# Kernel tuning notes

Hardware: AMD Instinct MI355X
Metric: run time of the kernel (lower is better)

The kernel has to match this reference:

```python
import jax, jax.numpy as jnp
import numpy as np

B = 128        # graph pairs per batch
NPG = 512      # nodes per graph (equal-size graphs -> dense batch is a reshape)
D = 64         # input feature dim
DEG = 16       # avg degree
FILTERS = [64, 32, 16]
RDIM = 10      # resize_dim
CCH = 8        # conv channels per similarity image
MLP = [32, 16, 8, 4, 1]


def _make_edges(rng, n_graphs, npg, deg):
    E = n_graphs * npg * deg
    off = np.repeat(np.arange(n_graphs, dtype=np.int64) * npg, npg * deg)
    src = rng.integers(0, npg, E) + off
    dst = rng.integers(0, npg, E) + off
    return jnp.asarray(np.stack([src, dst]), dtype=jnp.int32)


def setup_inputs() -> dict:
    key = jax.random.key(0)
    ks = jax.random.split(key, 40)
    rng = np.random.default_rng(0)
    N = B * NPG
    inp = {}
    inp['x_i'] = jax.random.normal(ks[0], (N, D), jnp.float32)
    inp['x_j'] = jax.random.normal(ks[1], (N, D), jnp.float32)
    # GCN weights
    dims = [D] + FILTERS
    k = 2
    for li in range(3):
        fi, fo = dims[li], dims[li + 1]
        inp[f'gcn_w{li}'] = jax.random.normal(ks[k], (fi, fo), jnp.float32) / np.sqrt(fi); k += 1
        inp[f'gcn_b{li}'] = jnp.zeros((fo,), jnp.float32)
    # Conv filters: one Conv2d(1->CCH, 3x3, SAME) per GNN layer, OIHW kernels
    for li in range(3):
        inp[f'conv_w{li}'] = jax.random.normal(ks[k], (CCH, 1, 3, 3), jnp.float32) / 3.0; k += 1
        inp[f'conv_b{li}'] = jnp.zeros((CCH,), jnp.float32)
    # MLP (Linear-ReLU stack) + scoring layer
    mdims = [3 * CCH * RDIM * RDIM] + MLP
    for li in range(len(MLP)):
        fi, fo = mdims[li], mdims[li + 1]
        inp[f'mlp_w{li}'] = jax.random.normal(ks[k], (fi, fo), jnp.float32) / np.sqrt(fi); k += 1
        inp[f'mlp_b{li}'] = jnp.zeros((fo,), jnp.float32)
    inp['score_w'] = jax.random.normal(ks[k], (1, 1), jnp.float32); k += 1
    inp['score_b'] = jnp.zeros((1,), jnp.float32)
    # Graph structure (int constants)
    inp['edge_index_i'] = _make_edges(rng, B, NPG, DEG)
    inp['edge_index_j'] = _make_edges(rng, B, NPG, DEG)
    batch = jnp.asarray(np.repeat(np.arange(B, dtype=np.int64), NPG), dtype=jnp.int32)
    inp['batch_i'] = batch
    inp['batch_j'] = batch
    return inp


def _gcn(x, ei, w, b):
    # PyG GCNConv: A_hat = D^-1/2 (A + I) D^-1/2 ; out = A_hat (x W) + b
    src, dst = ei[0], ei[1]
    n = x.shape[0]
    xw = x @ w
    deg = jax.ops.segment_sum(jnp.ones(ei.shape[1], xw.dtype), dst, num_segments=n) + 1.0
    inv = jax.lax.rsqrt(deg)
    msg = xw[src] * (inv[src] * inv[dst])[:, None]
    agg = jax.ops.segment_sum(msg, dst, num_segments=n)
    return agg + xw * (inv * inv)[:, None] + b


def _forward(x_i, x_j, gcn_w0, gcn_b0, gcn_w1, gcn_b1, gcn_w2, gcn_b2,
             conv_w0, conv_b0, conv_w1, conv_b1, conv_w2, conv_b2,
             mlp_w0, mlp_b0, mlp_w1, mlp_b1, mlp_w2, mlp_b2, mlp_w3, mlp_b3, mlp_w4, mlp_b4,
             score_w, score_b, edge_index_i, edge_index_j):
    gws = [(gcn_w0, gcn_b0), (gcn_w1, gcn_b1), (gcn_w2, gcn_b2)]
    cvs = [(conv_w0, conv_b0), (conv_w1, conv_b1), (conv_w2, conv_b2)]
    embs = []
    for li, (w, b) in enumerate(gws):
        x_i = _gcn(x_i, edge_index_i, w, b)
        x_j = _gcn(x_j, edge_index_j, w, b)
        if li != len(gws) - 1:  # activation + dropout (eval mode -> identity)
            x_i = jax.nn.relu(x_i)
            x_j = jax.nn.relu(x_j)
        h_i = x_i.reshape(B, NPG, -1)  # to_dense_batch (equal-size graphs)
        h_j = x_j.reshape(B, NPG, -1)
        sim = jnp.einsum('bnd,bmd->bnm', h_i, h_j)  # [B, NPG, NPG]
        simr = jax.image.resize(sim, (B, RDIM, RDIM), method='bilinear', antialias=False)
        cw, cb = cvs[li]
        y = jax.lax.conv_general_dilated(simr[:, None], cw, (1, 1), 'SAME')
        y = jax.nn.relu(y + cb[None, :, None, None])  # [B, CCH, RDIM, RDIM]
        embs.append(y.reshape(B, -1))
    feat = jnp.concatenate(embs, axis=1)  # [B, 3*CCH*RDIM*RDIM]
    for w, b in [(mlp_w0, mlp_b0), (mlp_w1, mlp_b1), (mlp_w2, mlp_b2), (mlp_w3, mlp_b3), (mlp_w4, mlp_b4)]:
        feat = jax.nn.relu(feat @ w + b)
    score = jax.nn.sigmoid(feat @ score_w + score_b)
    return score.reshape(-1)


def reference(x_i, x_j, gcn_w0, gcn_b0, gcn_w1, gcn_b1, gcn_w2, gcn_b2,
              conv_w0, conv_b0, conv_w1, conv_b1, conv_w2, conv_b2,
              mlp_w0, mlp_b0, mlp_w1, mlp_b1, mlp_w2, mlp_b2, mlp_w3, mlp_b3, mlp_w4, mlp_b4,
              score_w, score_b, edge_index_i, edge_index_j, batch_i, batch_j):
    # batch_i/batch_j are implicit in the block layout (equal-size graphs)
    return _forward(x_i, x_j, gcn_w0, gcn_b0, gcn_w1, gcn_b1, gcn_w2, gcn_b2,
                    conv_w0, conv_b0, conv_w1, conv_b1, conv_w2, conv_b2,
                    mlp_w0, mlp_b0, mlp_w1, mlp_b1, mlp_w2, mlp_b2, mlp_w3, mlp_b3, mlp_w4, mlp_b4,
                    score_w, score_b, edge_index_i, edge_index_j)
```

## Files before the change

### kernel.cpp

```cpp
#include <hip/hip_runtime.h>
#include <hip/hip_fp16.h>

typedef float fvec4 __attribute__((ext_vector_type(4)));
typedef int ivec4 __attribute__((ext_vector_type(4)));

#define NN 65536
#define EE 1048576
#define BB 128
#define NPG 512
#define EPG 8192

__device__ __forceinline__ int pkrtz(float a, float b) {
  union { __half2 h; int i; } u; u.h = __floats2half2_rn(a, b); return u.i;
}
__device__ __forceinline__ float2 up2(int v) {
  union { int i; __half2 h; } u; u.i = v; return __half22float2(u.h);
}

#define ACCQ(SA, SB, w) { float2 f_; \
  f_ = up2((w)[0]); (SA)[0] += f_.x; (SA)[1] += f_.y; \
  f_ = up2((w)[1]); (SA)[2] += f_.x; (SA)[3] += f_.y; \
  f_ = up2((w)[2]); (SB)[0] += f_.x; (SB)[1] += f_.y; \
  f_ = up2((w)[3]); (SB)[2] += f_.x; (SB)[3] += f_.y; }

__device__ __forceinline__ int slot_of(int node) {
  constexpr int srows[20] = {25, 26, 76, 77, 127, 128, 178, 179, 229, 230,
                             281, 282, 332, 333, 383, 384, 434, 435, 485, 486};
  int slot = -1;
#pragma unroll
  for (int i = 0; i < 20; ++i)
    if (node == srows[i]) slot = i;
  return slot;
}
__constant__ int c_srows[20] = {25, 26, 76, 77, 127, 128, 178, 179, 229, 230,
                                281, 282, 332, 333, 383, 384, 434, 435, 485, 486};

__global__ __launch_bounds__(512)
void kA(const float* __restrict__ x_i, const float* __restrict__ x_j,
        const float* __restrict__ gw0, const float* __restrict__ gb0,
        const float* __restrict__ gw1,
        const int* __restrict__ ei, const int* __restrict__ ej,
        unsigned short* __restrict__ sidsG, unsigned int* __restrict__ packG,
        float* __restrict__ hs0, unsigned int* __restrict__ y1G) {
  __shared__ ivec4 buf[NPG * 4];
  __shared__ unsigned short sids[EPG];
  __shared__ int cnt[NPG];
  __shared__ int posb[NPG];
  __shared__ int wsum[8];
  unsigned short* const dsts = reinterpret_cast<unsigned short*>(buf);

  const int bid = blockIdx.x;
  const int half = bid & 1;
  const int sg = bid >> 1;
  const int side = sg >> 7, g = sg & 127;
  const float* __restrict__ x = side ? x_j : x_i;
  const int* __restrict__ eidx = side ? ej : ei;
  const int v = threadIdx.x;
  const int base = g * NPG, ebase = g * EPG;

  cnt[v] = 0;
  __syncthreads();
  for (int k = v; k < EPG; k += 512) {
    int d = eidx[EE + ebase + k] - base;
    dsts[k] = (unsigned short)d;
    atomicAdd(&cnt[d], 1);
  }
  __syncthreads();

  const int count = cnt[v];
  int xa = count;
  const int lane = v & 63;
#pragma unroll
  for (int d = 1; d < 64; d <<= 1) {
    int y = __shfl_up(xa, d, 64);
    if (lane >= d) xa += y;
  }
  const int wid = v >> 6;
  if (lane == 63) wsum[wid] = xa;
  __syncthreads();
  if (v == 0) {
    int a = 0;
#pragma unroll
    for (int i = 0; i < 8; ++i) { int tv = wsum[i]; wsum[i] = a; a += tv; }
  }
  __syncthreads();
  posb[v] = xa - count + wsum[wid];
  __syncthreads();

  for (int k = v; k < EPG; k += 512) {
    int lv = eidx[ebase + k] - base;
    int p = atomicAdd(&posb[dsts[k]], 1);
    sids[p] = (unsigned short)lv;
  }

  fvec4 a0[8];
#pragma unroll
  for (int q = 0; q < 8; ++q) a0[q] = fvec4{0.f, 0.f, 0.f, 0.f};
  {
    const fvec4* xv = reinterpret_cast<const fvec4*>(x + (size_t)(base + v) * 64);
    const float* w0h = gw0 + half * 32;
#pragma unroll 1
    for (int k16 = 0; k16 < 4; ++k16) {
      fvec4 xq[4];
#pragma unroll
      for (int u = 0; u < 4; ++u) xq[u] = xv[4 * k16 + u];
#pragma unroll
      for (int u = 0; u < 4; ++u) {
#pragma unroll
        for (int j = 0; j < 4; ++j) {
          const float xk = xq[u][j];
          const fvec4* wr = reinterpret_cast<const fvec4*>(w0h + (size_t)(16 * k16 + 4 * u + j) * 64);
#pragma unroll
          for (int q = 0; q < 8; ++q) a0[q] += xk * wr[q];
        }
      }
    }
  }
  __syncthreads();

  const int sgE = sg * EPG;
  if (half == 0) {
    const int* srcI = reinterpret_cast<const int*>(sids);
    int* dstI = reinterpret_cast<int*>(sidsG + sgE);
    for (int k = v; k < EPG / 2; k += 512) dstI[k] = srcI[k];
    packG[sg * NPG + v] = ((unsigned int)(posb[v] - count) << 16) | (unsigned int)count;
  }
  const float inv_v = rsqrtf((float)count + 1.0f);
  const int myKey = (v << 2) | ((v >> 1) & 3);
  fvec4 s[8];
#pragma unroll
  for (int q = 0; q < 8; ++q) s[q] = a0[q] * inv_v;
#pragma unroll
  for (int q_ = 0; q_ < 4; ++q_) {
    ivec4 w_;
    w_[0] = pkrtz(s[2 * q_][0], s[2 * q_][1]);
    w_[1] = pkrtz(s[2 * q_][2], s[2 * q_][3]);
    w_[2] = pkrtz(s[2 * q_ + 1][0], s[2 * q_ + 1][1]);
    w_[3] = pkrtz(s[2 * q_ + 1][2], s[2 * q_ + 1][3]);
    buf[myKey ^ q_] = w_;
  }
  __syncthreads();

  const int nstart = posb[v] - count;
  {
    int e = nstart;
    const int end = nstart + count;
    for (; e + 2 <= end; e += 2) {
      const int la = sids[e], lb = sids[e + 1];
      const int Ka = (la << 2) | ((la >> 1) & 3);
      const int Kb = (lb << 2) | ((lb >> 1) & 3);
      const ivec4 a0_ = buf[Ka], a1_ = buf[Ka ^ 1], a2_ = buf[Ka ^ 2], a3_ = buf[Ka ^ 3];
      const ivec4 b0_ = buf[Kb], b1_ = buf[Kb ^ 1], b2_ = buf[Kb ^ 2], b3_ = buf[Kb ^ 3];
      ACCQ(s[0], s[1], a0_) ACCQ(s[2], s[3], a1_) ACCQ(s[4], s[5], a2_) ACCQ(s[6], s[7], a3_)
      ACCQ(s[0], s[1], b0_) ACCQ(s[2], s[3], b1_) ACCQ(s[4], s[5], b2_) ACCQ(s[6], s[7], b3_)
    }
    if (e < end) {
      const int la = sids[e];
      const int Ka = (la << 2) | ((la >> 1) & 3);
      const ivec4 a0_ = buf[Ka], a1_ = buf[Ka ^ 1], a2_ = buf[Ka ^ 2], a3_ = buf[Ka ^ 3];
      ACCQ(s[0], s[1], a0_) ACCQ(s[2], s[3], a1_) ACCQ(s[4], s[5], a2_) ACCQ(s[6], s[7], a3_)
    }
  }

  const int slot = slot_of(v);
  const int hb = (side * BB + g) * 20;
  fvec4 y1P[8];
#pragma unroll
  for (int p = 0; p < 8; ++p) y1P[p] = fvec4{0.f, 0.f, 0.f, 0.f};
  {
    const fvec4* gb0v = reinterpret_cast<const fvec4*>(gb0 + half * 32);
    fvec4* hp = reinterpret_cast<fvec4*>(hs0 + ((size_t)hb + slot) * 64 + half * 32);
#pragma unroll
    for (int q = 0; q < 8; ++q) {
      fvec4 o = s[q] * inv_v + gb0v[q];
#pragma unroll
      for (int j = 0; j < 4; ++j) o[j] = fmaxf(o[j], 0.f);
      if (slot >= 0) hp[q] = o;
#pragma unroll
      for (int j = 0; j < 4; ++j) {
        const float hf = o[j];
        const fvec4* wr = reinterpret_cast<const fvec4*>(gw1 + (size_t)(half * 32 + q * 4 + j) * 32);
#pragma unroll
        for (int p = 0; p < 8; ++p) y1P[p] += hf * wr[p];
      }
    }
  }
  {
    unsigned int* yp = y1G + ((size_t)(sg * 2 + half) * NPG + v) * 16;
#pragma unroll
    for (int w = 0; w < 16; ++w)
      yp[w] = (unsigned int)pkrtz(y1P[w >> 1][(w & 1) * 2], y1P[w >> 1][(w & 1) * 2 + 1]);
  }
}

__global__ __launch_bounds__(512)
void kB(const float* __restrict__ gb1, const float* __restrict__ gw2,
        const unsigned short* __restrict__ sidsG, const unsigned int* __restrict__ packG,
        const unsigned int* __restrict__ y1G,
        float* __restrict__ hs1, unsigned int* __restrict__ y2G) {
  __shared__ ivec4 buf[NPG * 2];
  __shared__ unsigned short sids[EPG];
  const int bid = blockIdx.x;
  const int half = bid & 1;
  const int sg = bid >> 1;
  const int side = sg >> 7, g = sg & 127;
  const int v = threadIdx.x;

  {
    const int* srcI = reinterpret_cast<const int*>(sidsG + sg * EPG);
    int* dstI = reinterpret_cast<int*>(sids);
    for (int k = v; k < EPG / 2; k += 512) dstI[k] = srcI[k];
  }
  const unsigned int pack = packG[sg * NPG + v];
  const int count = (int)(pack & 0xffffu);
  const int nstart = (int)(pack >> 16);
  const float inv_v = rsqrtf((float)count + 1.0f);

  fvec4 s1[4];
  {
    const unsigned int* p0 = y1G + ((size_t)(sg * 2 + 0) * NPG + v) * 16 + half * 8;
    const unsigned int* p1 = y1G + ((size_t)(sg * 2 + 1) * NPG + v) * 16 + half * 8;
#pragma unroll
    for (int w = 0; w < 8; ++w) {
      float2 fa = up2((int)p0[w]);
      float2 fb = up2((int)p1[w]);
      s1[w >> 1][(w & 1) * 2] = (fa.x + fb.x) * inv_v;
      s1[w >> 1][(w & 1) * 2 + 1] = (fa.y + fb.y) * inv_v;
    }
  }
  __syncthreads();
  const int myKey = (v << 1) | (v & 1);
  {
    ivec4 w0, w1;
    w0[0] = pkrtz(s1[0][0], s1[0][1]); w0[1] = pkrtz(s1[0][2], s1[0][3]);
    w0[2] = pkrtz(s1[1][0], s1[1][1]); w0[3] = pkrtz(s1[1][2], s1[1][3]);
    w1[0] = pkrtz(s1[2][0], s1[2][1]); w1[1] = pkrtz(s1[2][2], s1[2][3]);
    w1[2] = pkrtz(s1[3][0], s1[3][1]); w1[3] = pkrtz(s1[3][2], s1[3][3]);
    buf[myKey] = w0;
    buf[myKey ^ 1] = w1;
  }
  __syncthreads();

  {
    int e = nstart;
    const int end = nstart + count;
    for (; e + 2 <= end; e += 2) {
      const int la = sids[e], lb = sids[e + 1];
      const int Ka = (la << 1) | (la & 1), Kb = (lb << 1) | (lb & 1);
      const ivec4 a0_ = buf[Ka], a1_ = buf[Ka ^ 1];
      const ivec4 b0_ = buf[Kb], b1_ = buf[Kb ^ 1];
      ACCQ(s1[0], s1[1], a0_) ACCQ(s1[2], s1[3], a1_)
      ACCQ(s1[0], s1[1], b0_) ACCQ(s1[2], s1[3], b1_)
    }
    if (e < end) {
      const int la = sids[e];
      const int Ka = (la << 1) | (la & 1);
      const ivec4 a0_ = buf[Ka], a1_ = buf[Ka ^ 1];
      ACCQ(s1[0], s1[1], a0_) ACCQ(s1[2], s1[3], a1_)
    }
  }

  const int slot = slot_of(v);
  const int hb = (side * BB + g) * 20;
  fvec4 y2P[4];
#pragma unroll
  for (int p = 0; p < 4; ++p) y2P[p] = fvec4{0.f, 0.f, 0.f, 0.f};
  {
    const fvec4* gb1v = reinterpret_cast<const fvec4*>(gb1 + half * 16);
    fvec4* hp = reinterpret_cast<fvec4*>(hs1 + ((size_t)hb + slot) * 32 + half * 16);
#pragma unroll
    for (int q = 0; q < 4; ++q) {
      fvec4 o = s1[q] * inv_v + gb1v[q];
#pragma unroll
      for (int j = 0; j < 4; ++j) o[j] = fmaxf(o[j], 0.f);
      if (slot >= 0) hp[q] = o;
#pragma unroll
      for (int j = 0; j < 4; ++j) {
        const float hf = o[j];
        const fvec4* wr = reinterpret_cast<const fvec4*>(gw2 + (size_t)(half * 16 + q * 4 + j) * 16);
#pragma unroll
        for (int p = 0; p < 4; ++p) y2P[p] += hf * wr[p];
      }
    }
  }
  {
    unsigned int* yp = y2G + ((size_t)(sg * 2 + half) * NPG + v) * 8;
#pragma unroll
    for (int w = 0; w < 8; ++w)
      yp[w] = (unsigned int)pkrtz(y2P[w >> 1][(w & 1) * 2], y2P[w >> 1][(w & 1) * 2 + 1]);
  }
}

__global__ __launch_bounds__(512)
void kC(const float* __restrict__ gb2,
        const unsigned short* __restrict__ sidsG, const unsigned int* __restrict__ packG,
        const unsigned int* __restrict__ y2G, float* __restrict__ hs2) {
  __shared__ ivec4 buf[NPG * 2];
  __shared__ unsigned short sids[EPG];
  const int sg = blockIdx.x;
  const int side = sg >> 7, g = sg & 127;
  const int v = threadIdx.x;

  {
    const int* srcI = reinterpret_cast<const int*>(sidsG + sg * EPG);
    int* dstI = reinterpret_cast<int*>(sids);
    for (int k = v; k < EPG / 2; k += 512) dstI[k] = srcI[k];
  }
  const unsigned int pack = packG[sg * NPG + v];
  const int count = (int)(pack & 0xffffu);
  const float inv_v = rsqrtf((float)count + 1.0f);

  const int myKey = (v << 1) | (v & 1);
  {
    const unsigned int* p0 = y2G + ((size_t)(sg * 2 + 0) * NPG + v) * 8;
    const unsigned int* p1 = y2G + ((size_t)(sg * 2 + 1) * NPG + v) * 8;
    fvec4 y2[4];
#pragma unroll
    for (int w = 0; w < 8; ++w) {
      float2 fa = up2((int)p0[w]);
      float2 fb = up2((int)p1[w]);
      y2[w >> 1][(w & 1) * 2] = (fa.x + fb.x) * inv_v;
      y2[w >> 1][(w & 1) * 2 + 1] = (fa.y + fb.y) * inv_v;
    }
    ivec4 w0, w1;
    w0[0] = pkrtz(y2[0][0], y2[0][1]); w0[1] = pkrtz(y2[0][2], y2[0][3]);
    w0[2] = pkrtz(y2[1][0], y2[1][1]); w0[3] = pkrtz(y2[1][2], y2[1][3]);
    w1[0] = pkrtz(y2[2][0], y2[2][1]); w1[1] = pkrtz(y2[2][2], y2[2][3]);
    w1[2] = pkrtz(y2[3][0], y2[3][1]); w1[3] = pkrtz(y2[3][2], y2[3][3]);
    buf[myKey] = w0;
    buf[myKey ^ 1] = w1;
  }
  __syncthreads();

  if (v < 20) {
    const int n = c_srows[v];
    const unsigned int cp = packG[sg * NPG + n];
    const int ccount = (int)(cp & 0xffffu);
    const int cstart = (int)(cp >> 16);
    const float cinv = rsqrtf((float)ccount + 1.0f);
    const int ckey = (n << 1) | (n & 1);
    fvec4 s2[4];
#pragma unroll
    for (int q = 0; q < 4; ++q) s2[q] = fvec4{0.f, 0.f, 0.f, 0.f};
    {
      const ivec4 w0 = buf[ckey], w1 = buf[ckey ^ 1];
      ACCQ(s2[0], s2[1], w0) ACCQ(s2[2], s2[3], w1)
    }
    for (int e = cstart; e < cstart + ccount; ++e) {
      const int la = sids[e];
      const int Ka = (la << 1) | (la & 1);
      const ivec4 w0 = buf[Ka], w1 = buf[Ka ^ 1];
      ACCQ(s2[0], s2[1], w0) ACCQ(s2[2], s2[3], w1)
    }
    const int hb = (side * BB + g) * 20;
    const fvec4* gb2v = reinterpret_cast<const fvec4*>(gb2);
    fvec4* hp = reinterpret_cast<fvec4*>(hs2 + ((size_t)hb + v) * 16);
#pragma unroll
    for (int q = 0; q < 4; ++q) hp[q] = s2[q] * cinv + gb2v[q];
  }
}

__global__ __launch_bounds__(256) void k_head(const float* __restrict__ hs0, const float* __restrict__ hs1,
                                              const float* __restrict__ hs2,
                                              const float* __restrict__ cw0, const float* __restrict__ cb0,
                                              const float* __restrict__ cw1, const float* __restrict__ cb1,
                                              const float* __restrict__ cw2, const float* __restrict__ cb2,
                                              const float* __restrict__ mw0, const float* __restrict__ mb0,
                                              const float* __restrict__ mw1, const float* __restrict__ mb1,
                                              const float* __restrict__ mw2, const float* __restrict__ mb2,
                                              const float* __restrict__ mw3, const float* __restrict__ mb3,
                                              const float* __restrict__ mw4, const float* __restrict__ mb4,
                                              const float* __restrict__ sw, const float* __restrict__ sb,
                                              float* __restrict__ out) {
  __shared__ float hi[2240];
  __shared__ float hj[2240];
  __shared__ float sim[400];
  __shared__ float simr[100];
  __shared__ float feat[2400];
  __shared__ float red[256];
  __shared__ float mbuf[60];
  const int b = blockIdx.x, t = threadIdx.x;

  for (int k = t; k < 1280; k += 256) {
    hi[k] = hs0[(size_t)(0 * BB + b) * 1280 + k];
    hj[k] = hs0[(size_t)(1 * BB + b) * 1280 + k];
  }
  for (int k = t; k < 640; k += 256) {
    hi[1280 + k] = hs1[(size_t)(0 * BB + b) * 640 + k];
    hj[1280 + k] = hs1[(size_t)(1 * BB + b) * 640 + k];
  }
  for (int k = t; k < 320; k += 256) {
    hi[1920 + k] = hs2[(size_t)(0 * BB + b) * 320 + k];
    hj[1920 + k] = hs2[(size_t)(1 * BB + b) * 320 + k];
  }
  __syncthreads();

  const int Fs[3] = {64, 32, 16};
  const int HOFF[3] = {0, 1280, 1920};
  const float* CW[3] = {cw0, cw1, cw2};
  const float* CB[3] = {cb0, cb1, cb2};

  for (int li = 0; li < 3; ++li) {
    const int F = Fs[li];
    const float* Hi = hi + HOFF[li];
    const float* Hj = hj + HOFF[li];
    for (int p = t; p < 400; p += 256) {
      int r = p / 20, cq = p % 20;
      float a = 0.0f;
      for (int d = 0; d < F; ++d) a += Hi[r * F + d] * Hj[cq * F + d];
      sim[p] = a;
    }
    __syncthreads();
    if (t < 100) {
      int oy = t / 10, ox = t % 10;
      float cy = (oy + 0.5f) * (512.0f / 10.0f) - 0.5f;
      float cx = (ox + 0.5f) * (512.0f / 10.0f) - 0.5f;
      float fy = cy - floorf(cy);
      float fx = cx - floorf(cx);
      int r0 = 2 * oy, c0 = 2 * ox;
      float s00 = sim[r0 * 20 + c0], s01 = sim[r0 * 20 + c0 + 1];
      float s10 = sim[(r0 + 1) * 20 + c0], s11 = sim[(r0 + 1) * 20 + c0 + 1];
      simr[t] = (1.0f - fy) * ((1.0f - fx) * s00 + fx * s01) + fy * ((1.0f - fx) * s10 + fx * s11);
    }
    __syncthreads();
    const float* cw = CW[li];
    const float* cb = CB[li];
    for (int idx = t; idx < 800; idx += 256) {
      int cch = idx / 100, rem = idx % 100, y = rem / 10, x = rem % 10;
      float a = cb[cch];
#pragma unroll
      for (int ky = 0; ky < 3; ++ky) {
#pragma unroll
        for (int kx = 0; kx < 3; ++kx) {
          int iy = y + ky - 1, ix = x + kx - 1;
          if (iy >= 0 && iy < 10 && ix >= 0 && ix < 10)
            a += cw[cch * 9 + ky * 3 + kx] * simr[iy * 10 + ix];
        }
      }
      feat[li * 800 + idx] = fmaxf(a, 0.0f);
    }
    __syncthreads();
  }

  {
    int f = t & 31, part = t >> 5;
    float a = 0.0f;
    int k0 = part * 300;
    for (int k = k0; k < k0 + 300; ++k) a += feat[k] * mw0[k * 32 + f];
    red[t] = a;
    __syncthreads();
    if (t < 32) {
      float s = mb0[t];
#pragma unroll
      for (int p = 0; p < 8; ++p) s += red[p * 32 + t];
      mbuf[t] = fmaxf(s, 0.0f);
    }
    __syncthreads();
  }
  if (t < 16) {
    float s = mb1[t];
    for (int k = 0; k < 32; ++k) s += mbuf[k] * mw1[k * 16 + t];
    mbuf[32 + t] = fmaxf(s, 0.0f);
  }
  __syncthreads();
  if (t < 8) {
    float s = mb2[t];
    for (int k = 0; k < 16; ++k) s += mbuf[32 + k] * mw2[k * 8 + t];
    mbuf[48 + t] = fmaxf(s, 0.0f);
  }
  __syncthreads();
  if (t < 4) {
    float s = mb3[t];
    for (int k = 0; k < 8; ++k) s += mbuf[48 + k] * mw3[k * 4 + t];
    mbuf[56 + t] = fmaxf(s, 0.0f);
  }
  __syncthreads();
  if (t == 0) {
    float s = mb4[0];
    for (int k = 0; k < 4; ++k) s += mbuf[56 + k] * mw4[k];
    s = fmaxf(s, 0.0f);
    float z = s * sw[0] + sb[0];
    out[b] = 1.0f / (1.0f + expf(-z));
  }
}

extern "C" void kernel_launch(void* const* d_in, const int* in_sizes, int n_in,
                              void* d_out, int out_size, void* d_ws, size_t ws_size,
                              hipStream_t stream) {
  (void)in_sizes; (void)n_in; (void)out_size; (void)ws_size;
  const float* x_i = (const float*)d_in[0];
  const float* x_j = (const float*)d_in[1];
  const float* gw0 = (const float*)d_in[2];
  const float* gb0 = (const float*)d_in[3];
  const float* gw1 = (const float*)d_in[4];
  const float* gb1 = (const float*)d_in[5];
  const float* gw2 = (const float*)d_in[6];
  const float* gb2 = (const float*)d_in[7];
  const float* cw0 = (const float*)d_in[8];
  const float* cb0 = (const float*)d_in[9];
  const float* cw1 = (const float*)d_in[10];
  const float* cb1 = (const float*)d_in[11];
  const float* cw2 = (const float*)d_in[12];
  const float* cb2 = (const float*)d_in[13];
  const float* mw0 = (const float*)d_in[14];
  const float* mb0 = (const float*)d_in[15];
  const float* mw1 = (const float*)d_in[16];
  const float* mb1 = (const float*)d_in[17];
  const float* mw2 = (const float*)d_in[18];
  const float* mb2 = (const float*)d_in[19];
  const float* mw3 = (const float*)d_in[20];
  const float* mb3 = (const float*)d_in[21];
  const float* mw4 = (const float*)d_in[22];
  const float* mb4 = (const float*)d_in[23];
  const float* scw = (const float*)d_in[24];
  const float* scb = (const float*)d_in[25];
  const int* ei = (const int*)d_in[26];
  const int* ej = (const int*)d_in[27];
  float* out = (float*)d_out;

  char* p = (char*)d_ws;
  auto take = [&](size_t bytes) {
    char* r = p;
    p += (bytes + 255) & ~(size_t)255;
    return r;
  };
  float* hs0 = (float*)take((size_t)2 * BB * 20 * 64 * 4);
  float* hs1 = (float*)take((size_t)2 * BB * 20 * 32 * 4);
  float* hs2 = (float*)take((size_t)2 * BB * 20 * 16 * 4);
  unsigned short* sidsG = (unsigned short*)take((size_t)2 * BB * EPG * 2);
  unsigned int* packG = (unsigned int*)take((size_t)2 * BB * NPG * 4);
  unsigned int* y1G = (unsigned int*)take((size_t)2 * BB * 2 * NPG * 16 * 4);
  unsigned int* y2G = (unsigned int*)take((size_t)2 * BB * 2 * NPG * 8 * 4);

  kA<<<2 * BB * 2, 512, 0, stream>>>(x_i, x_j, gw0, gb0, gw1, ei, ej,
                                     sidsG, packG, hs0, y1G);
  kB<<<2 * BB * 2, 512, 0, stream>>>(gb1, gw2, sidsG, packG, y1G, hs1, y2G);
  kC<<<2 * BB, 512, 0, stream>>>(gb2, sidsG, packG, y2G, hs2);
  k_head<<<BB, 256, 0, stream>>>(hs0, hs1, hs2, cw0, cb0, cw1, cb1, cw2, cb2,
                                 mw0, mb0, mw1, mb1, mw2, mb2, mw3, mb3, mw4, mb4,
                                 scw, scb, out);
}
```

Measured before the change: 121.6 us.

## Split CSR edge-sort into a separate preprocessing kernel shared by both halves

Graph CSR construction (degree count, scan, bucket scatter) moves out of kA into a new kP kernel launched once per graph instead of once per half-block. kA then loads the sorted source ids and degree packs from global memory, as kB and kC already do. This removes the duplicated sort work across the two feature halves, at the cost of an extra kernel launch and a global round-trip. A barrier in kB before the shared-buffer write is also removed.

Measured after the change: 124.2 us. 2.1% more time.

```diff
diff --git a/kernel.cpp b/kernel.cpp
--- a/kernel.cpp
+++ b/kernel.cpp
@@ -36,62 +36,87 @@
                                 281, 282, 332, 333, 383, 384, 434, 435, 485, 486};
 
 __global__ __launch_bounds__(512)
-void kA(const float* __restrict__ x_i, const float* __restrict__ x_j,
-        const float* __restrict__ gw0, const float* __restrict__ gb0,
-        const float* __restrict__ gw1,
-        const int* __restrict__ ei, const int* __restrict__ ej,
-        unsigned short* __restrict__ sidsG, unsigned int* __restrict__ packG,
-        float* __restrict__ hs0, unsigned int* __restrict__ y1G) {
-  __shared__ ivec4 buf[NPG * 4];
+void kP(const int* __restrict__ ei, const int* __restrict__ ej,
+        unsigned short* __restrict__ sidsG, unsigned int* __restrict__ packG) {
+  __shared__ unsigned short dsts[EPG];
   __shared__ unsigned short sids[EPG];
   __shared__ int cnt[NPG];
   __shared__ int posb[NPG];
   __shared__ int wsum[8];
-  unsigned short* const dsts = reinterpret_cast<unsigned short*>(buf);
-
+  const int sg = blockIdx.x;
+  const int side = sg >> 7, g = sg & 127;
+  const int* __restrict__ eidx = side ? ej : ei;
+  const int v = threadIdx.x;
+  const int base = g * NPG, ebase = g * EPG;
+
+  cnt[v] = 0;
+  __syncthreads();
+  for (int k = v; k < EPG; k += 512) {
+    int d = eidx[EE + ebase + k] - base;
+    dsts[k] = (unsigned short)d;
+    atomicAdd(&cnt[d], 1);
+  }
+  __syncthreads();
+
+  const int count = cnt[v];
+  int xa = count;
+  const int lane = v & 63;
+#pragma unroll
+  for (int d = 1; d < 64; d <<= 1) {
+    int y = __shfl_up(xa, d, 64);
+    if (lane >= d) xa += y;
+  }
+  const int wid = v >> 6;
+  if (lane == 63) wsum[wid] = xa;
+  __syncthreads();
+  if (v == 0) {
+    int a = 0;
+#pragma unroll
+    for (int i = 0; i < 8; ++i) { int tv = wsum[i]; wsum[i] = a; a += tv; }
+  }
+  __syncthreads();
+  const int start = xa - count + wsum[wid];
+  posb[v] = start;
+  packG[sg * NPG + v] = ((unsigned int)start << 16) | (unsigned int)count;
+  __syncthreads();
+
+  for (int k = v; k < EPG; k += 512) {
+    int lv = eidx[ebase + k] - base;
+    int p = atomicAdd(&posb[dsts[k]], 1);
+    sids[p] = (unsigned short)lv;
+  }
+  __syncthreads();
+
+  const int* srcI = reinterpret_cast<const int*>(sids);
+  int* dstI = reinterpret_cast<int*>(sidsG + (size_t)sg * EPG);
+  for (int k = v; k < EPG / 2; k += 512) dstI[k] = srcI[k];
+}
+
+__global__ __launch_bounds__(512)
+void kA(const float* __restrict__ x_i, const float* __restrict__ x_j,
+        const float* __restrict__ gw0, const float* __restrict__ gb0,
+        const float* __restrict__ gw1,
+        const unsigned short* __restrict__ sidsG, const unsigned int* __restrict__ packG,
+        float* __restrict__ hs0, unsigned int* __restrict__ y1G) {
+  __shared__ ivec4 buf[NPG * 4];
+  __shared__ unsigned short sids[EPG];
   const int bid = blockIdx.x;
   const int half = bid & 1;
   const int sg = bid >> 1;
   const int side = sg >> 7, g = sg & 127;
   const float* __restrict__ x = side ? x_j : x_i;
-  const int* __restrict__ eidx = side ? ej : ei;
   const int v = threadIdx.x;
-  const int base = g * NPG, ebase = g * EPG;
-
-  cnt[v] = 0;
-  __syncthreads();
-  for (int k = v; k < EPG; k += 512) {
-    int d = eidx[EE + ebase + k] - base;
-    dsts[k] = (unsigned short)d;
-    atomicAdd(&cnt[d], 1);
-  }
-  __syncthreads();
-
-  const int count = cnt[v];
-  int xa = count;
-  const int lane = v & 63;
-#pragma unroll
-  for (int d = 1; d < 64; d <<= 1) {
-    int y = __shfl_up(xa, d, 64);
-    if (lane >= d) xa += y;
-  }
-  const int wid = v >> 6;
-  if (lane == 63) wsum[wid] = xa;
-  __syncthreads();
-  if (v == 0) {
-    int a = 0;
-#pragma unroll
-    for (int i = 0; i < 8; ++i) { int tv = wsum[i]; wsum[i] = a; a += tv; }
-  }
-  __syncthreads();
-  posb[v] = xa - count + wsum[wid];
-  __syncthreads();
-
-  for (int k = v; k < EPG; k += 512) {
-    int lv = eidx[ebase + k] - base;
-    int p = atomicAdd(&posb[dsts[k]], 1);
-    sids[p] = (unsigned short)lv;
-  }
+  const int base = g * NPG;
+
+  {
+    const int* srcI = reinterpret_cast<const int*>(sidsG + (size_t)sg * EPG);
+    int* dstI = reinterpret_cast<int*>(sids);
+    for (int k = v; k < EPG / 2; k += 512) dstI[k] = srcI[k];
+  }
+  const unsigned int pack = packG[sg * NPG + v];
+  const int count = (int)(pack & 0xffffu);
+  const int nstart = (int)(pack >> 16);
+  const float inv_v = rsqrtf((float)count + 1.0f);
 
   fvec4 a0[8];
 #pragma unroll
@@ -116,16 +141,7 @@
       }
     }
   }
-  __syncthreads();
-
-  const int sgE = sg * EPG;
-  if (half == 0) {
-    const int* srcI = reinterpret_cast<const int*>(sids);
-    int* dstI = reinterpret_cast<int*>(sidsG + sgE);
-    for (int k = v; k < EPG / 2; k += 512) dstI[k] = srcI[k];
-    packG[sg * NPG + v] = ((unsigned int)(posb[v] - count) << 16) | (unsigned int)count;
-  }
-  const float inv_v = rsqrtf((float)count + 1.0f);
+
   const int myKey = (v << 2) | ((v >> 1) & 3);
   fvec4 s[8];
 #pragma unroll
@@ -141,7 +157,6 @@
   }
   __syncthreads();
 
-  const int nstart = posb[v] - count;
   {
     int e = nstart;
     const int end = nstart + count;
@@ -207,7 +222,7 @@
   const int v = threadIdx.x;
 
   {
-    const int* srcI = reinterpret_cast<const int*>(sidsG + sg * EPG);
+    const int* srcI = reinterpret_cast<const int*>(sidsG + (size_t)sg * EPG);
     int* dstI = reinterpret_cast<int*>(sids);
     for (int k = v; k < EPG / 2; k += 512) dstI[k] = srcI[k];
   }
@@ -228,7 +243,6 @@
       s1[w >> 1][(w & 1) * 2 + 1] = (fa.y + fb.y) * inv_v;
     }
   }
-  __syncthreads();
   const int myKey = (v << 1) | (v & 1);
   {
     ivec4 w0, w1;
@@ -302,7 +316,7 @@
   const int v = threadIdx.x;
 
   {
-    const int* srcI = reinterpret_cast<const int*>(sidsG + sg * EPG);
+    const int* srcI = reinterpret_cast<const int*>(sidsG + (size_t)sg * EPG);
     int* dstI = reinterpret_cast<int*>(sids);
     for (int k = v; k < EPG / 2; k += 512) dstI[k] = srcI[k];
   }
@@ -532,7 +546,8 @@
   unsigned int* y1G = (unsigned int*)take((size_t)2 * BB * 2 * NPG * 16 * 4);
   unsigned int* y2G = (unsigned int*)take((size_t)2 * BB * 2 * NPG * 8 * 4);
 
-  kA<<<2 * BB * 2, 512, 0, stream>>>(x_i, x_j, gw0, gb0, gw1, ei, ej,
+  kP<<<2 * BB, 512, 0, stream>>>(ei, ej, sidsG, packG);
+  kA<<<2 * BB * 2, 512, 0, stream>>>(x_i, x_j, gw0, gb0, gw1,
                                      sidsG, packG, hs0, y1G);
   kB<<<2 * BB * 2, 512, 0, stream>>>(gb1, gw2, sidsG, packG, y1G, hs1, y2G);
   kC<<<2 * BB, 512, 0, stream>>>(gb2, sidsG, packG, y2G, hs2);
```
